# Performance work log

Hardware: AMD Instinct MI355X
Metric: run time of the kernel (lower is better)

Reference implementation:

```python
import jax, jax.numpy as jnp
import numpy as np

# Constants matching init_kwargs
FEATURE_DIM = 512
QK_DIM = 128
GATE_VALUE = 0.2
TOPK = 32
TEMP = QK_DIM ** (-0.5)


def _l2norm(x, eps=1e-12):
    # F.normalize(p=2, dim=-1): x / max(||x||_2, eps)
    return x / jnp.maximum(jnp.linalg.norm(x, axis=-1, keepdims=True), eps)


def setup_inputs() -> dict:
    key = jax.random.key(0)
    ks = jax.random.split(key, 6)
    B, Nq, Nk = 64, 512, 2048  # Nq == FEATURE_DIM (required by the gather/residual shapes)
    query = jax.random.normal(ks[0], (B, Nq, FEATURE_DIM), dtype=jnp.float32)
    key_feat = jax.random.normal(ks[1], (B, Nk, FEATURE_DIM // 2), dtype=jnp.float32)
    value = jax.random.normal(ks[2], (B, Nk, FEATURE_DIM // 2), dtype=jnp.float32)
    # torch.nn.Linear weights are [out, in]; init N(0, sqrt(2/out_features))
    WQ = jax.random.normal(ks[3], (QK_DIM, FEATURE_DIM), dtype=jnp.float32) * np.sqrt(2.0 / QK_DIM).astype(np.float32)
    WK = jax.random.normal(ks[4], (QK_DIM, FEATURE_DIM // 2), dtype=jnp.float32) * np.sqrt(2.0 / QK_DIM).astype(np.float32)
    WV = jax.random.normal(ks[5], (FEATURE_DIM, FEATURE_DIM // 2), dtype=jnp.float32) * np.sqrt(2.0 / FEATURE_DIM).astype(np.float32)
    return {"query": query, "key_feat": key_feat, "value": value, "WQ": WQ, "WK": WK, "WV": WV}


def reference(query, key_feat, value, WQ, WK, WV):
    # Projections (Linear, no bias) + L2 normalize
    w_q = _l2norm(jnp.einsum('bqf,df->bqd', query, WQ))        # [B, Nq, Dqk]
    w_k = _l2norm(jnp.einsum('bkf,df->bkd', key_feat, WK))     # [B, Nk, Dqk]
    dot_prod = jnp.einsum('bqd,bkd->bqk', w_q, w_k)            # [B, Nq, Nk]
    mask = jnp.max(dot_prod, axis=2) > GATE_VALUE              # [B, Nq] bool
    affinity = jax.nn.softmax(dot_prod * TEMP, axis=-1)        # [B, Nq, Nk]
    topk_vals, topk_idx = jax.lax.top_k(affinity, TOPK)        # [B, Nq, TOPK]
    w_v = _l2norm(jnp.einsum('bkf,cf->bkc', value, WV))        # [B, Nk, F]
    # Faithful torch.gather semantics: index permuted to [B, TOPK, Nq];
    # sel[b,t,c] = w_v[b, topk_idx[b,c,t], c]  (per-channel gather, needs Nq == F)
    sel = jnp.take_along_axis(w_v, jnp.swapaxes(topk_idx, 1, 2), axis=1)  # [B, TOPK, F]
    gather = jnp.einsum('bqt,btc->bqc', topk_vals, sel)        # [B, Nq, F]
    return gather * mask[:, :, None].astype(gather.dtype) + query
```

## Files before the change

### kernel.cpp

```cpp
#include <hip/hip_runtime.h>
#include <math.h>

#define NB   64
#define NQ   512
#define NK   2048
#define FD   512
#define FH   256
#define DQ   128
#define KTOP 32
#define GATEV 0.2f
#define TEMPF 0.08838834764831843f

typedef __attribute__((ext_vector_type(8))) short bf16x8;
typedef __attribute__((ext_vector_type(4))) float f32x4;

__device__ __forceinline__ unsigned short f32_bf16_rne(float f) {
    unsigned u = __float_as_uint(f);
    u += 0x7FFFu + ((u >> 16) & 1u);
    return (unsigned short)(u >> 16);
}
__device__ __forceinline__ unsigned short bf16_orderable(unsigned short b) {
    return (unsigned short)(b ^ ((b & 0x8000u) ? 0xFFFFu : 0x8000u));
}
__device__ __forceinline__ float ord_to_f32(unsigned u) {
    unsigned m = (u & 0x8000u) ? 0x8000u : 0xFFFFu;
    return __uint_as_float((u ^ m) << 16);
}
__device__ __forceinline__ float key_value(unsigned key) {
    return ord_to_f32((key >> 11) & 0xFFFFu);
}
__device__ __forceinline__ float exp_small(float y) {
    return 1.f + y * (1.f + y * (0.5f + y * (0.16666667f + y * 0.041666668f)));
}
__device__ __forceinline__ bf16x8 cvt8(const float* p) {
    float4 a = ((const float4*)p)[0];
    float4 b = ((const float4*)p)[1];
    bf16x8 o;
    o[0] = (short)f32_bf16_rne(a.x); o[1] = (short)f32_bf16_rne(a.y);
    o[2] = (short)f32_bf16_rne(a.z); o[3] = (short)f32_bf16_rne(a.w);
    o[4] = (short)f32_bf16_rne(b.x); o[5] = (short)f32_bf16_rne(b.y);
    o[6] = (short)f32_bf16_rne(b.z); o[7] = (short)f32_bf16_rne(b.w);
    return o;
}
__device__ __forceinline__ unsigned umaxu(unsigned a, unsigned b) { return a > b ? a : b; }
__device__ __forceinline__ unsigned uminu(unsigned a, unsigned b) { return a < b ? a : b; }

__global__ __launch_bounds__(256) void kW_cvt(const float* __restrict__ WQ,
                                              const float* __restrict__ WK,
                                              const float* __restrict__ WV,
                                              unsigned short* __restrict__ wqW,
                                              unsigned short* __restrict__ wkW,
                                              unsigned short* __restrict__ wvb) {
    const int i = blockIdx.x * 256 + threadIdx.x;
    if (i < 65536) wqW[i] = f32_bf16_rne(WQ[i]);
    else if (i < 98304) wkW[i - 65536] = f32_bf16_rne(WK[i - 65536]);
    else wvb[i - 98304] = f32_bf16_rne(WV[i - 98304]);
}

template<int K>
__global__ __launch_bounds__(256) void kProj(const float* __restrict__ X,
                                             const unsigned short* __restrict__ Wb,
                                             unsigned short* __restrict__ outb) {
    constexpr int M     = (K == 256) ? 2 : 1;
    constexpr int NS    = K / 32;
    constexpr int GPR   = K / 8;
    constexpr int CROWS = 32768 / K;
    constexpr int NCHK  = 128 / CROWS;
    constexpr int CTC   = 8 / NCHK;
    __shared__ __attribute__((aligned(16))) unsigned short wchunk[CROWS * K];
    const int tid = threadIdx.x, wave = tid >> 6, lane = tid & 63;
    const int rt = lane & 15, kg = lane >> 4;
    const size_t rowbase = (size_t)blockIdx.x * (64 * M) + wave * (16 * M);

    bf16x8 afr[M][NS];
#pragma unroll
    for (int m = 0; m < M; ++m) {
        const float* xrow = X + (rowbase + m * 16 + rt) * K;
#pragma unroll
        for (int s = 0; s < NS; ++s) afr[m][s] = cvt8(xrow + kg * 8 + s * 32);
    }

    if constexpr (K == 256) {
#pragma unroll
        for (int it = 0; it < 16; ++it) {
            int idx = it * 256 + tid;
            int cl = idx / GPR, g = idx % GPR;
            *(bf16x8*)(wchunk + (cl * GPR + (g ^ (cl & 7))) * 8) =
                *(const bf16x8*)(Wb + (size_t)cl * K + g * 8);
        }
        __syncthreads();
        float nrm[M][4];
#pragma unroll
        for (int m = 0; m < M; ++m)
#pragma unroll
            for (int r = 0; r < 4; ++r) nrm[m][r] = 0.f;
#pragma unroll 1
        for (int ct = 0; ct < 8; ++ct) {
            const int cl = ct * 16 + rt;
#pragma unroll
            for (int m = 0; m < M; ++m) {
                f32x4 acc = {0.f, 0.f, 0.f, 0.f};
#pragma unroll
                for (int s = 0; s < NS; ++s) {
                    int gr = cl * GPR + ((s * 4 + kg) ^ (cl & 7));
                    bf16x8 bfr = *(const bf16x8*)(wchunk + gr * 8);
                    acc = __builtin_amdgcn_mfma_f32_16x16x32_bf16(afr[m][s], bfr, acc, 0, 0, 0);
                }
#pragma unroll
                for (int r = 0; r < 4; ++r) nrm[m][r] += acc[r] * acc[r];
            }
        }
#pragma unroll
        for (int o = 1; o < 16; o <<= 1) {
#pragma unroll
            for (int m = 0; m < M; ++m)
#pragma unroll
                for (int r = 0; r < 4; ++r) nrm[m][r] += __shfl_xor(nrm[m][r], o);
        }
        float inv[M][4];
#pragma unroll
        for (int m = 0; m < M; ++m)
#pragma unroll
            for (int r = 0; r < 4; ++r) inv[m][r] = 1.f / fmaxf(sqrtf(nrm[m][r]), 1e-12f);
#pragma unroll 1
        for (int ct = 0; ct < 8; ++ct) {
            const int cl = ct * 16 + rt;
#pragma unroll
            for (int m = 0; m < M; ++m) {
                f32x4 acc = {0.f, 0.f, 0.f, 0.f};
#pragma unroll
                for (int s = 0; s < NS; ++s) {
                    int gr = cl * GPR + ((s * 4 + kg) ^ (cl & 7));
                    bf16x8 bfr = *(const bf16x8*)(wchunk + gr * 8);
                    acc = __builtin_amdgcn_mfma_f32_16x16x32_bf16(afr[m][s], bfr, acc, 0, 0, 0);
                }
#pragma unroll
                for (int r = 0; r < 4; ++r)
                    outb[(rowbase + m * 16 + kg * 4 + r) * DQ + ct * 16 + rt] =
                        f32_bf16_rne(acc[r] * inv[m][r]);
            }
        }
    } else {
        f32x4 acc[8];
#pragma unroll
        for (int j = 0; j < 8; ++j) acc[j] = (f32x4){0.f, 0.f, 0.f, 0.f};
#pragma unroll
        for (int ch = 0; ch < NCHK; ++ch) {
            __syncthreads();
#pragma unroll
            for (int it = 0; it < 16; ++it) {
                int idx = it * 256 + tid;
                int cl = idx / GPR, g = idx % GPR;
                *(bf16x8*)(wchunk + (cl * GPR + (g ^ (cl & 7))) * 8) =
                    *(const bf16x8*)(Wb + (size_t)(ch * CROWS + cl) * K + g * 8);
            }
            __syncthreads();
#pragma unroll 1
            for (int ct = 0; ct < CTC; ++ct) {
                const int cl = ct * 16 + rt;
                const int jg = ch * CTC + ct;
#pragma unroll
                for (int s = 0; s < NS; ++s) {
                    int gr = cl * GPR + ((s * 4 + kg) ^ (cl & 7));
                    bf16x8 bfr = *(const bf16x8*)(wchunk + gr * 8);
                    acc[jg] = __builtin_amdgcn_mfma_f32_16x16x32_bf16(afr[0][s], bfr, acc[jg], 0, 0, 0);
                }
            }
        }
        float nrm[4];
#pragma unroll
        for (int r = 0; r < 4; ++r) {
            float s = 0.f;
#pragma unroll
            for (int j = 0; j < 8; ++j) s += acc[j][r] * acc[j][r];
            nrm[r] = s;
        }
#pragma unroll
        for (int o = 1; o < 16; o <<= 1) {
#pragma unroll
            for (int r = 0; r < 4; ++r) nrm[r] += __shfl_xor(nrm[r], o);
        }
        float inv[4];
#pragma unroll
        for (int r = 0; r < 4; ++r) inv[r] = 1.f / fmaxf(sqrtf(nrm[r]), 1e-12f);
#pragma unroll
        for (int j = 0; j < 8; ++j) {
#pragma unroll
            for (int r = 0; r < 4; ++r)
                outb[(rowbase + kg * 4 + r) * DQ + j * 16 + rt] = f32_bf16_rne(acc[j][r] * inv[r]);
        }
    }
}

__global__ __launch_bounds__(256) void kC2_vnorm(const float* __restrict__ value,
                                                 const unsigned short* __restrict__ wvb,
                                                 float* __restrict__ invnv) {
    __shared__ __attribute__((aligned(16))) unsigned short wchunk[128 * 256];
    const int tid = threadIdx.x, wave = tid >> 6, lane = tid & 63;
    const int rt = lane & 15, kg = lane >> 4;
    const size_t rowbase = (size_t)blockIdx.x * 128 + wave * 32;

    bf16x8 afr[2][8];
#pragma unroll
    for (int m = 0; m < 2; ++m) {
        const float* vrow = value + (rowbase + m * 16 + rt) * FH;
#pragma unroll
        for (int s = 0; s < 8; ++s) afr[m][s] = cvt8(vrow + kg * 8 + s * 32);
    }
    float nrm[2][4] = {{0.f, 0.f, 0.f, 0.f}, {0.f, 0.f, 0.f, 0.f}};

    for (int ch = 0; ch < 4; ++ch) {
        __syncthreads();
        const unsigned short* src = wvb + (size_t)ch * 128 * FH;
#pragma unroll
        for (int it = 0; it < 16; ++it) {
            int idx = it * 256 + tid;
            int c_local = idx >> 5, g = idx & 31;
            int dst = c_local * 32 + (g ^ (c_local & 7));
            *(bf16x8*)(wchunk + dst * 8) = *(const bf16x8*)(src + (size_t)c_local * FH + g * 8);
        }
        __syncthreads();
#pragma unroll 1
        for (int ct = 0; ct < 8; ++ct) {
            const int cl = ct * 16 + rt;
            f32x4 acc0 = {0.f, 0.f, 0.f, 0.f}, acc1 = {0.f, 0.f, 0.f, 0.f};
#pragma unroll
            for (int s = 0; s < 8; ++s) {
                int gr = cl * 32 + ((s * 4 + kg) ^ (cl & 7));
                bf16x8 bfr = *(const bf16x8*)(wchunk + gr * 8);
                acc0 = __builtin_amdgcn_mfma_f32_16x16x32_bf16(afr[0][s], bfr, acc0, 0, 0, 0);
                acc1 = __builtin_amdgcn_mfma_f32_16x16x32_bf16(afr[1][s], bfr, acc1, 0, 0, 0);
            }
#pragma unroll
            for (int r = 0; r < 4; ++r) {
                nrm[0][r] += acc0[r] * acc0[r];
                nrm[1][r] += acc1[r] * acc1[r];
            }
        }
    }
#pragma unroll
    for (int o = 1; o < 16; o <<= 1) {
#pragma unroll
        for (int m = 0; m < 2; ++m)
#pragma unroll
            for (int r = 0; r < 4; ++r) nrm[m][r] += __shfl_xor(nrm[m][r], o);
    }
    if (rt == 0) {
#pragma unroll
        for (int m = 0; m < 2; ++m)
#pragma unroll
            for (int r = 0; r < 4; ++r)
                invnv[rowbase + m * 16 + kg * 4 + r] = 1.f / fmaxf(sqrtf(nrm[m][r]), 1e-12f);
    }
}

__global__ __launch_bounds__(512) void kD_fused(const unsigned short* __restrict__ wqb,
                                                const unsigned short* __restrict__ wkb,
                                                float* __restrict__ vals,
                                                int* __restrict__ idxs,
                                                float* __restrict__ maskf) {
    __shared__ unsigned cand[64][128];
    __shared__ float sums[64][8];
    const int tid = threadIdx.x, wave = tid >> 6, lane = tid & 63;
    const int rt = lane & 15, kg = lane >> 4;
    const int wid = (blockIdx.x & 7) * 64 + (blockIdx.x >> 3);
    const int b = wid >> 3;
    const size_t qrow0 = (size_t)b * NQ + (wid & 7) * 64;

    bf16x8 afr[4][4];
#pragma unroll
    for (int m = 0; m < 4; ++m) {
        const unsigned short* aq = wqb + (qrow0 + m * 16 + rt) * DQ + kg * 8;
#pragma unroll
        for (int s = 0; s < 4; ++s) afr[m][s] = *(const bf16x8*)(aq + s * 32);
    }

    const unsigned short* bk0 = wkb + ((size_t)b * NK + wave * 256 + rt) * DQ + kg * 8;
    unsigned best[4][4];
    float sum4[4][4];
#pragma unroll
    for (int m = 0; m < 4; ++m)
#pragma unroll
        for (int r = 0; r < 4; ++r) { best[m][r] = 0u; sum4[m][r] = 0.f; }

#pragma unroll 2
    for (int kt = 0; kt < 16; ++kt) {
        const unsigned short* bk = bk0 + (size_t)kt * 16 * DQ;
        bf16x8 bfr[4];
#pragma unroll
        for (int s = 0; s < 4; ++s) bfr[s] = *(const bf16x8*)(bk + s * 32);
        const unsigned idc = 2047u - (unsigned)(wave * 256 + kt * 16 + rt);
#pragma unroll
        for (int m = 0; m < 4; ++m) {
            f32x4 acc = {0.f, 0.f, 0.f, 0.f};
#pragma unroll
            for (int s = 0; s < 4; ++s)
                acc = __builtin_amdgcn_mfma_f32_16x16x32_bf16(afr[m][s], bfr[s], acc, 0, 0, 0);
#pragma unroll
            for (int r = 0; r < 4; ++r) {
                unsigned short u = bf16_orderable(f32_bf16_rne(acc[r]));
                best[m][r] = umaxu(best[m][r], ((unsigned)u << 11) | idc);
                sum4[m][r] += exp_small(acc[r] * TEMPF);
            }
        }
    }
#pragma unroll
    for (int o = 1; o < 16; o <<= 1) {
#pragma unroll
        for (int m = 0; m < 4; ++m)
#pragma unroll
            for (int r = 0; r < 4; ++r) sum4[m][r] += __shfl_xor(sum4[m][r], o);
    }
#pragma unroll
    for (int m = 0; m < 4; ++m)
#pragma unroll
        for (int r = 0; r < 4; ++r) cand[m * 16 + kg * 4 + r][wave * 16 + rt] = best[m][r];
    if (rt == 0) {
#pragma unroll
        for (int m = 0; m < 4; ++m)
#pragma unroll
            for (int r = 0; r < 4; ++r) sums[m * 16 + kg * 4 + r][wave] = sum4[m][r];
    }
    __syncthreads();

#pragma unroll 1
    for (int rr = 0; rr < 8; ++rr) {
        const int row = wave * 8 + rr;
        float sA = sums[row][lane & 7];
#pragma unroll
        for (int o = 1; o < 8; o <<= 1) sA += __shfl_xor(sA, o);
        const float invA = 1.f / sA;

        unsigned c0 = umaxu(cand[row][lane], cand[row][lane + 64]);
#pragma unroll
        for (int kq = 2; kq <= 64; kq <<= 1) {
#pragma unroll
            for (int jj = kq >> 1; jj > 0; jj >>= 1) {
                unsigned x0 = __shfl_xor(c0, jj);
                const bool keepmax = (((lane & jj) == 0) ^ ((lane & kq) != 0));
                c0 = keepmax ? umaxu(c0, x0) : uminu(c0, x0);
            }
        }
        const float maxv0 = key_value(__shfl((int)c0, 0));
        if (lane == 0) maskf[qrow0 + row] = (maxv0 > GATEV) ? 1.f : 0.f;
        if (lane < KTOP) {
            const size_t gr0 = (qrow0 + row) * KTOP;
            vals[gr0 + lane] = exp_small(key_value(c0) * TEMPF) * invA;
            idxs[gr0 + lane] = (int)(2047u - (c0 & 0x7FFu));
        }
    }
}

__global__ __launch_bounds__(256) void kE_sel(const float* __restrict__ value,
                                              const float* __restrict__ WV,
                                              const float* __restrict__ invnv,
                                              const int* __restrict__ idxs,
                                              unsigned short* __restrict__ selT) {
    __shared__ __attribute__((aligned(16))) float wvc[FH];
    __shared__ int id_s[KTOP];
    const int tid = threadIdx.x;
    const int wid = (blockIdx.x & 7) * 4096 + (blockIdx.x >> 3);
    const int b = wid >> 9;
    const int c = wid & 511;
    wvc[tid] = WV[(size_t)c * FH + tid];
    if (tid < KTOP) id_s[tid] = idxs[((size_t)b * NQ + c) * KTOP + tid];
    __syncthreads();
    const int t = tid >> 3;
    const int l8 = tid & 7;
    const int k = id_s[t];
    const float4* v4 = (const float4*)(value + ((size_t)b * NK + k) * FH);
    const float4* w4 = (const float4*)wvc;
    float s = 0.f;
#pragma unroll
    for (int m = 0; m < 8; ++m) {
        float4 a = v4[l8 + 8 * m];
        float4 w = w4[l8 + 8 * m];
        s += a.x * w.x + a.y * w.y + a.z * w.z + a.w * w.w;
    }
#pragma unroll
    for (int o = 4; o > 0; o >>= 1) s += __shfl_down(s, o, 8);
    if (l8 == 0)
        selT[((size_t)b * FD + c) * KTOP + t] = f32_bf16_rne(s * invnv[(size_t)b * NK + k]);
}

__global__ __launch_bounds__(256) void kF_out(const float* __restrict__ vals,
                                              const unsigned short* __restrict__ selT,
                                              const float* __restrict__ maskf,
                                              const float* __restrict__ query,
                                              float* __restrict__ out) {
    const int tid = threadIdx.x, wave = tid >> 6, lane = tid & 63;
    const int rt = lane & 15, kg = lane >> 4;
    const int b = blockIdx.x >> 5;
    const int q0 = (blockIdx.x & 31) * 16;
    const int cbase = wave * 128;

    bf16x8 afr = cvt8(vals + ((size_t)b * NQ + q0 + rt) * KTOP + kg * 8);
    f32x4 acc[8];
#pragma unroll
    for (int ct = 0; ct < 8; ++ct) {
        bf16x8 bfr = *(const bf16x8*)(selT + ((size_t)b * FD + cbase + ct * 16 + rt) * KTOP + kg * 8);
        acc[ct] = __builtin_amdgcn_mfma_f32_16x16x32_bf16(afr, bfr, (f32x4){0.f,0.f,0.f,0.f}, 0, 0, 0);
    }
    float m[4];
#pragma unroll
    for (int r = 0; r < 4; ++r) m[r] = maskf[(size_t)b * NQ + q0 + kg * 4 + r];
#pragma unroll
    for (int ct = 0; ct < 8; ++ct) {
#pragma unroll
        for (int r = 0; r < 4; ++r) {
            const size_t off = ((size_t)b * NQ + q0 + kg * 4 + r) * FD + cbase + ct * 16 + rt;
            out[off] = fmaf(m[r], acc[ct][r], query[off]);
        }
    }
}

extern "C" void kernel_launch(void* const* d_in, const int* in_sizes, int n_in,
                              void* d_out, int out_size, void* d_ws, size_t ws_size,
                              hipStream_t stream) {
    (void)in_sizes; (void)n_in; (void)out_size; (void)ws_size;
    const float* query = (const float*)d_in[0];
    const float* keyf  = (const float*)d_in[1];
    const float* value = (const float*)d_in[2];
    const float* WQ    = (const float*)d_in[3];
    const float* WK    = (const float*)d_in[4];
    const float* WV    = (const float*)d_in[5];
    float* out = (float*)d_out;

    unsigned short* wqb = (unsigned short*)d_ws;
    unsigned short* wkb = wqb + (size_t)NB * NQ * DQ;
    unsigned short* wvb = wkb + (size_t)NB * NK * DQ;
    unsigned short* wqW = wvb + (size_t)FD * FH;
    unsigned short* wkW = wqW + (size_t)DQ * FD;
    float* invnv = (float*)(wkW + (size_t)DQ * FH);
    float* vals  = invnv + (size_t)NB * NK;
    int*   idxs  = (int*)(vals + (size_t)NB * NQ * KTOP);
    float* maskf = (float*)(idxs + (size_t)NB * NQ * KTOP);
    unsigned short* selT = (unsigned short*)(maskf + (size_t)NB * NQ);

    kW_cvt<<<dim3(896), dim3(256), 0, stream>>>(WQ, WK, WV, wqW, wkW, wvb);
    kProj<512><<<dim3(NB * NQ / 64), dim3(256), 0, stream>>>(query, wqW, wqb);
    kProj<256><<<dim3(NB * NK / 128), dim3(256), 0, stream>>>(keyf, wkW, wkb);
    kC2_vnorm<<<dim3(NB * NK / 128), dim3(256), 0, stream>>>(value, wvb, invnv);
    kD_fused<<<dim3(512), dim3(512), 0, stream>>>(wqb, wkb, vals, idxs, maskf);
    kE_sel<<<dim3(NB * FD), dim3(256), 0, stream>>>(value, WV, invnv, idxs, selT);
    kF_out<<<dim3(NB * 32), dim3(256), 0, stream>>>(vals, selT, maskf, query, out);
}
```

Baseline: 282.9 us.

## Merge weight conversion and three projection kernels into one interleaved launch

Folds the fp32-to-bf16 weight conversion into the projection bodies and merges the Q projection, K projection and value-norm kernels into a single kernel. Block IDs are interleaved so Q, K and V work run concurrently across the grid. This removes three kernel launches and their serialization tails, plus the intermediate bf16 weight buffers. In exchange, every block re-converts its weight chunk from fp32, which doubles weight bytes read per block and adds conversion ALU work. The heterogeneous branches also share one shared-memory allocation size.

```diff
diff --git a/kernel.cpp b/kernel.cpp
--- a/kernel.cpp
+++ b/kernel.cpp
@@ -45,161 +45,149 @@
 __device__ __forceinline__ unsigned umaxu(unsigned a, unsigned b) { return a > b ? a : b; }
 __device__ __forceinline__ unsigned uminu(unsigned a, unsigned b) { return a < b ? a : b; }
 
-__global__ __launch_bounds__(256) void kW_cvt(const float* __restrict__ WQ,
-                                              const float* __restrict__ WK,
-                                              const float* __restrict__ WV,
-                                              unsigned short* __restrict__ wqW,
-                                              unsigned short* __restrict__ wkW,
-                                              unsigned short* __restrict__ wvb) {
-    const int i = blockIdx.x * 256 + threadIdx.x;
-    if (i < 65536) wqW[i] = f32_bf16_rne(WQ[i]);
-    else if (i < 98304) wkW[i - 65536] = f32_bf16_rne(WK[i - 65536]);
-    else wvb[i - 98304] = f32_bf16_rne(WV[i - 98304]);
-}
-
-template<int K>
-__global__ __launch_bounds__(256) void kProj(const float* __restrict__ X,
-                                             const unsigned short* __restrict__ Wb,
-                                             unsigned short* __restrict__ outb) {
-    constexpr int M     = (K == 256) ? 2 : 1;
-    constexpr int NS    = K / 32;
-    constexpr int GPR   = K / 8;
-    constexpr int CROWS = 32768 / K;
-    constexpr int NCHK  = 128 / CROWS;
-    constexpr int CTC   = 8 / NCHK;
-    __shared__ __attribute__((aligned(16))) unsigned short wchunk[CROWS * K];
-    const int tid = threadIdx.x, wave = tid >> 6, lane = tid & 63;
+
+__device__ __forceinline__ void body_projQ(int bid, int tid,
+                                           const float* __restrict__ X,
+                                           const float* __restrict__ Wf,
+                                           unsigned short* __restrict__ outb,
+                                           unsigned short* wchunk) {
+    const int wave = tid >> 6, lane = tid & 63;
     const int rt = lane & 15, kg = lane >> 4;
-    const size_t rowbase = (size_t)blockIdx.x * (64 * M) + wave * (16 * M);
-
-    bf16x8 afr[M][NS];
-#pragma unroll
-    for (int m = 0; m < M; ++m) {
-        const float* xrow = X + (rowbase + m * 16 + rt) * K;
-#pragma unroll
-        for (int s = 0; s < NS; ++s) afr[m][s] = cvt8(xrow + kg * 8 + s * 32);
-    }
-
-    if constexpr (K == 256) {
+    const size_t rowbase = (size_t)bid * 64 + wave * 16;
+    const float* xrow = X + (rowbase + rt) * 512;
+    bf16x8 afr[16];
+#pragma unroll
+    for (int s = 0; s < 16; ++s) afr[s] = cvt8(xrow + kg * 8 + s * 32);
+    f32x4 acc[8];
+#pragma unroll
+    for (int j = 0; j < 8; ++j) acc[j] = (f32x4){0.f, 0.f, 0.f, 0.f};
+#pragma unroll
+    for (int ch = 0; ch < 2; ++ch) {
+        __syncthreads();
 #pragma unroll
         for (int it = 0; it < 16; ++it) {
             int idx = it * 256 + tid;
-            int cl = idx / GPR, g = idx % GPR;
-            *(bf16x8*)(wchunk + (cl * GPR + (g ^ (cl & 7))) * 8) =
-                *(const bf16x8*)(Wb + (size_t)cl * K + g * 8);
+            int cl = idx >> 6, g = idx & 63;
+            *(bf16x8*)(wchunk + (cl * 64 + (g ^ (cl & 7))) * 8) =
+                cvt8(Wf + (size_t)(ch * 64 + cl) * 512 + g * 8);
         }
         __syncthreads();
-        float nrm[M][4];
-#pragma unroll
-        for (int m = 0; m < M; ++m)
-#pragma unroll
-            for (int r = 0; r < 4; ++r) nrm[m][r] = 0.f;
 #pragma unroll 1
-        for (int ct = 0; ct < 8; ++ct) {
+        for (int ct = 0; ct < 4; ++ct) {
             const int cl = ct * 16 + rt;
-#pragma unroll
-            for (int m = 0; m < M; ++m) {
-                f32x4 acc = {0.f, 0.f, 0.f, 0.f};
-#pragma unroll
-                for (int s = 0; s < NS; ++s) {
-                    int gr = cl * GPR + ((s * 4 + kg) ^ (cl & 7));
-                    bf16x8 bfr = *(const bf16x8*)(wchunk + gr * 8);
-                    acc = __builtin_amdgcn_mfma_f32_16x16x32_bf16(afr[m][s], bfr, acc, 0, 0, 0);
-                }
-#pragma unroll
-                for (int r = 0; r < 4; ++r) nrm[m][r] += acc[r] * acc[r];
-            }
-        }
-#pragma unroll
-        for (int o = 1; o < 16; o <<= 1) {
-#pragma unroll
-            for (int m = 0; m < M; ++m)
-#pragma unroll
-                for (int r = 0; r < 4; ++r) nrm[m][r] += __shfl_xor(nrm[m][r], o);
-        }
-        float inv[M][4];
-#pragma unroll
-        for (int m = 0; m < M; ++m)
-#pragma unroll
-            for (int r = 0; r < 4; ++r) inv[m][r] = 1.f / fmaxf(sqrtf(nrm[m][r]), 1e-12f);
+            const int jg = ch * 4 + ct;
+#pragma unroll
+            for (int s = 0; s < 16; ++s) {
+                int gr = cl * 64 + ((s * 4 + kg) ^ (cl & 7));
+                bf16x8 bfr = *(const bf16x8*)(wchunk + gr * 8);
+                acc[jg] = __builtin_amdgcn_mfma_f32_16x16x32_bf16(afr[s], bfr, acc[jg], 0, 0, 0);
+            }
+        }
+    }
+    float nrm[4];
+#pragma unroll
+    for (int r = 0; r < 4; ++r) {
+        float s = 0.f;
+#pragma unroll
+        for (int j = 0; j < 8; ++j) s += acc[j][r] * acc[j][r];
+        nrm[r] = s;
+    }
+#pragma unroll
+    for (int o = 1; o < 16; o <<= 1) {
+#pragma unroll
+        for (int r = 0; r < 4; ++r) nrm[r] += __shfl_xor(nrm[r], o);
+    }
+    float inv[4];
+#pragma unroll
+    for (int r = 0; r < 4; ++r) inv[r] = 1.f / fmaxf(sqrtf(nrm[r]), 1e-12f);
+#pragma unroll
+    for (int j = 0; j < 8; ++j) {
+#pragma unroll
+        for (int r = 0; r < 4; ++r)
+            outb[(rowbase + kg * 4 + r) * DQ + j * 16 + rt] = f32_bf16_rne(acc[j][r] * inv[r]);
+    }
+}
+
+__device__ __forceinline__ void body_projK(int bid, int tid,
+                                           const float* __restrict__ X,
+                                           const float* __restrict__ Wf,
+                                           unsigned short* __restrict__ outb,
+                                           unsigned short* wchunk) {
+    const int wave = tid >> 6, lane = tid & 63;
+    const int rt = lane & 15, kg = lane >> 4;
+    const size_t rowbase = (size_t)bid * 128 + wave * 32;
+    bf16x8 afr[2][8];
+#pragma unroll
+    for (int m = 0; m < 2; ++m) {
+        const float* xrow = X + (rowbase + m * 16 + rt) * 256;
+#pragma unroll
+        for (int s = 0; s < 8; ++s) afr[m][s] = cvt8(xrow + kg * 8 + s * 32);
+    }
+#pragma unroll
+    for (int it = 0; it < 16; ++it) {
+        int idx = it * 256 + tid;
+        int cl = idx >> 5, g = idx & 31;
+        *(bf16x8*)(wchunk + (cl * 32 + (g ^ (cl & 7))) * 8) =
+            cvt8(Wf + (size_t)cl * 256 + g * 8);
+    }
+    __syncthreads();
+    float nrm[2][4] = {{0.f,0.f,0.f,0.f},{0.f,0.f,0.f,0.f}};
 #pragma unroll 1
-        for (int ct = 0; ct < 8; ++ct) {
-            const int cl = ct * 16 + rt;
-#pragma unroll
-            for (int m = 0; m < M; ++m) {
-                f32x4 acc = {0.f, 0.f, 0.f, 0.f};
-#pragma unroll
-                for (int s = 0; s < NS; ++s) {
-                    int gr = cl * GPR + ((s * 4 + kg) ^ (cl & 7));
-                    bf16x8 bfr = *(const bf16x8*)(wchunk + gr * 8);
-                    acc = __builtin_amdgcn_mfma_f32_16x16x32_bf16(afr[m][s], bfr, acc, 0, 0, 0);
-                }
-#pragma unroll
-                for (int r = 0; r < 4; ++r)
-                    outb[(rowbase + m * 16 + kg * 4 + r) * DQ + ct * 16 + rt] =
-                        f32_bf16_rne(acc[r] * inv[m][r]);
-            }
-        }
-    } else {
-        f32x4 acc[8];
-#pragma unroll
-        for (int j = 0; j < 8; ++j) acc[j] = (f32x4){0.f, 0.f, 0.f, 0.f};
-#pragma unroll
-        for (int ch = 0; ch < NCHK; ++ch) {
-            __syncthreads();
-#pragma unroll
-            for (int it = 0; it < 16; ++it) {
-                int idx = it * 256 + tid;
-                int cl = idx / GPR, g = idx % GPR;
-                *(bf16x8*)(wchunk + (cl * GPR + (g ^ (cl & 7))) * 8) =
-                    *(const bf16x8*)(Wb + (size_t)(ch * CROWS + cl) * K + g * 8);
-            }
-            __syncthreads();
+    for (int ct = 0; ct < 8; ++ct) {
+        const int cl = ct * 16 + rt;
+#pragma unroll
+        for (int m = 0; m < 2; ++m) {
+            f32x4 acc = {0.f, 0.f, 0.f, 0.f};
+#pragma unroll
+            for (int s = 0; s < 8; ++s) {
+                int gr = cl * 32 + ((s * 4 + kg) ^ (cl & 7));
+                bf16x8 bfr = *(const bf16x8*)(wchunk + gr * 8);
+                acc = __builtin_amdgcn_mfma_f32_16x16x32_bf16(afr[m][s], bfr, acc, 0, 0, 0);
+            }
+#pragma unroll
+            for (int r = 0; r < 4; ++r) nrm[m][r] += acc[r] * acc[r];
+        }
+    }
+#pragma unroll
+    for (int o = 1; o < 16; o <<= 1) {
+#pragma unroll
+        for (int m = 0; m < 2; ++m)
+#pragma unroll
+            for (int r = 0; r < 4; ++r) nrm[m][r] += __shfl_xor(nrm[m][r], o);
+    }
+    float inv[2][4];
+#pragma unroll
+    for (int m = 0; m < 2; ++m)
+#pragma unroll
+        for (int r = 0; r < 4; ++r) inv[m][r] = 1.f / fmaxf(sqrtf(nrm[m][r]), 1e-12f);
 #pragma unroll 1
-            for (int ct = 0; ct < CTC; ++ct) {
-                const int cl = ct * 16 + rt;
-                const int jg = ch * CTC + ct;
-#pragma unroll
-                for (int s = 0; s < NS; ++s) {
-                    int gr = cl * GPR + ((s * 4 + kg) ^ (cl & 7));
-                    bf16x8 bfr = *(const bf16x8*)(wchunk + gr * 8);
-                    acc[jg] = __builtin_amdgcn_mfma_f32_16x16x32_bf16(afr[0][s], bfr, acc[jg], 0, 0, 0);
-                }
-            }
-        }
-        float nrm[4];
-#pragma unroll
-        for (int r = 0; r < 4; ++r) {
-            float s = 0.f;
-#pragma unroll
-            for (int j = 0; j < 8; ++j) s += acc[j][r] * acc[j][r];
-            nrm[r] = s;
-        }
-#pragma unroll
-        for (int o = 1; o < 16; o <<= 1) {
-#pragma unroll
-            for (int r = 0; r < 4; ++r) nrm[r] += __shfl_xor(nrm[r], o);
-        }
-        float inv[4];
-#pragma unroll
-        for (int r = 0; r < 4; ++r) inv[r] = 1.f / fmaxf(sqrtf(nrm[r]), 1e-12f);
-#pragma unroll
-        for (int j = 0; j < 8; ++j) {
+    for (int ct = 0; ct < 8; ++ct) {
+        const int cl = ct * 16 + rt;
+#pragma unroll
+        for (int m = 0; m < 2; ++m) {
+            f32x4 acc = {0.f, 0.f, 0.f, 0.f};
+#pragma unroll
+            for (int s = 0; s < 8; ++s) {
+                int gr = cl * 32 + ((s * 4 + kg) ^ (cl & 7));
+                bf16x8 bfr = *(const bf16x8*)(wchunk + gr * 8);
+                acc = __builtin_amdgcn_mfma_f32_16x16x32_bf16(afr[m][s], bfr, acc, 0, 0, 0);
+            }
 #pragma unroll
             for (int r = 0; r < 4; ++r)
-                outb[(rowbase + kg * 4 + r) * DQ + j * 16 + rt] = f32_bf16_rne(acc[j][r] * inv[r]);
-        }
-    }
-}
-
-__global__ __launch_bounds__(256) void kC2_vnorm(const float* __restrict__ value,
-                                                 const unsigned short* __restrict__ wvb,
-                                                 float* __restrict__ invnv) {
-    __shared__ __attribute__((aligned(16))) unsigned short wchunk[128 * 256];
-    const int tid = threadIdx.x, wave = tid >> 6, lane = tid & 63;
+                outb[(rowbase + m * 16 + kg * 4 + r) * DQ + ct * 16 + rt] =
+                    f32_bf16_rne(acc[r] * inv[m][r]);
+        }
+    }
+}
+
+__device__ __forceinline__ void body_c2(int bid, int tid,
+                                        const float* __restrict__ value,
+                                        const float* __restrict__ WVf,
+                                        float* __restrict__ invnv,
+                                        unsigned short* wchunk) {
+    const int wave = tid >> 6, lane = tid & 63;
     const int rt = lane & 15, kg = lane >> 4;
-    const size_t rowbase = (size_t)blockIdx.x * 128 + wave * 32;
-
+    const size_t rowbase = (size_t)bid * 128 + wave * 32;
     bf16x8 afr[2][8];
 #pragma unroll
     for (int m = 0; m < 2; ++m) {
@@ -207,23 +195,21 @@
 #pragma unroll
         for (int s = 0; s < 8; ++s) afr[m][s] = cvt8(vrow + kg * 8 + s * 32);
     }
-    float nrm[2][4] = {{0.f, 0.f, 0.f, 0.f}, {0.f, 0.f, 0.f, 0.f}};
-
+    float nrm[2][4] = {{0.f,0.f,0.f,0.f},{0.f,0.f,0.f,0.f}};
     for (int ch = 0; ch < 4; ++ch) {
         __syncthreads();
-        const unsigned short* src = wvb + (size_t)ch * 128 * FH;
 #pragma unroll
         for (int it = 0; it < 16; ++it) {
             int idx = it * 256 + tid;
-            int c_local = idx >> 5, g = idx & 31;
-            int dst = c_local * 32 + (g ^ (c_local & 7));
-            *(bf16x8*)(wchunk + dst * 8) = *(const bf16x8*)(src + (size_t)c_local * FH + g * 8);
+            int cl = idx >> 5, g = idx & 31;
+            *(bf16x8*)(wchunk + (cl * 32 + (g ^ (cl & 7))) * 8) =
+                cvt8(WVf + (size_t)(ch * 128 + cl) * FH + g * 8);
         }
         __syncthreads();
 #pragma unroll 1
         for (int ct = 0; ct < 8; ++ct) {
             const int cl = ct * 16 + rt;
-            f32x4 acc0 = {0.f, 0.f, 0.f, 0.f}, acc1 = {0.f, 0.f, 0.f, 0.f};
+            f32x4 acc0 = {0.f,0.f,0.f,0.f}, acc1 = {0.f,0.f,0.f,0.f};
 #pragma unroll
             for (int s = 0; s < 8; ++s) {
                 int gr = cl * 32 + ((s * 4 + kg) ^ (cl & 7));
@@ -252,6 +238,23 @@
             for (int r = 0; r < 4; ++r)
                 invnv[rowbase + m * 16 + kg * 4 + r] = 1.f / fmaxf(sqrtf(nrm[m][r]), 1e-12f);
     }
+}
+
+__global__ __launch_bounds__(256) void kPre(const float* __restrict__ query,
+                                            const float* __restrict__ keyf,
+                                            const float* __restrict__ value,
+                                            const float* __restrict__ WQ,
+                                            const float* __restrict__ WK,
+                                            const float* __restrict__ WV,
+                                            unsigned short* __restrict__ wqb,
+                                            unsigned short* __restrict__ wkb,
+                                            float* __restrict__ invnv) {
+    __shared__ __attribute__((aligned(16))) unsigned short wchunk[32768];
+    const int tid = threadIdx.x;
+    const int g5 = blockIdx.x / 5, r5 = blockIdx.x % 5;
+    if (r5 == 0)      body_projQ(g5, tid, query, WQ, wqb, wchunk);
+    else if (r5 <= 2) body_projK(g5 * 2 + (r5 - 1), tid, keyf, WK, wkb, wchunk);
+    else              body_c2(g5 * 2 + (r5 - 3), tid, value, WV, invnv, wchunk);
 }
 
 __global__ __launch_bounds__(512) void kD_fused(const unsigned short* __restrict__ wqb,
@@ -428,19 +431,14 @@
 
     unsigned short* wqb = (unsigned short*)d_ws;
     unsigned short* wkb = wqb + (size_t)NB * NQ * DQ;
-    unsigned short* wvb = wkb + (size_t)NB * NK * DQ;
-    unsigned short* wqW = wvb + (size_t)FD * FH;
-    unsigned short* wkW = wqW + (size_t)DQ * FD;
-    float* invnv = (float*)(wkW + (size_t)DQ * FH);
+    float* invnv = (float*)(wkb + (size_t)NB * NK * DQ);
     float* vals  = invnv + (size_t)NB * NK;
     int*   idxs  = (int*)(vals + (size_t)NB * NQ * KTOP);
     float* maskf = (float*)(idxs + (size_t)NB * NQ * KTOP);
     unsigned short* selT = (unsigned short*)(maskf + (size_t)NB * NQ);
 
-    kW_cvt<<<dim3(896), dim3(256), 0, stream>>>(WQ, WK, WV, wqW, wkW, wvb);
-    kProj<512><<<dim3(NB * NQ / 64), dim3(256), 0, stream>>>(query, wqW, wqb);
-    kProj<256><<<dim3(NB * NK / 128), dim3(256), 0, stream>>>(keyf, wkW, wkb);
-    kC2_vnorm<<<dim3(NB * NK / 128), dim3(256), 0, stream>>>(value, wvb, invnv);
+    kPre<<<dim3(2560), dim3(256), 0, stream>>>(query, keyf, value, WQ, WK, WV,
+                                               wqb, wkb, invnv);
     kD_fused<<<dim3(512), dim3(512), 0, stream>>>(wqb, wkb, vals, idxs, maskf);
     kE_sel<<<dim3(NB * FD), dim3(256), 0, stream>>>(value, WV, invnv, idxs, selT);
     kF_out<<<dim3(NB * 32), dim3(256), 0, stream>>>(vals, selT, maskf, query, out);
```

Result: slower. 288.8 us (+2.1%).
